# Performance work log

Hardware: AMD Instinct MI355X
Metric: run time of the kernel (lower is better)

The kernel has to match this reference:

```python
import jax, jax.numpy as jnp
import numpy as np

# ---- static config (mirrors init_kwargs) ----
N_DIM = 3                      # manifold dimension n
D_COMP = 6                     # n(n+1)/2 metric components
M_PER = (12, 12, 12)           # HSGP basis functions per dim
M_STAR = 12 * 12 * 12          # 1728
T_STEPS = 50                   # time points in linspace(0,1,t)
C_SCALE = 1.5                  # HSGP domain scaling c
BATCH = 8192
ROWS = np.array([0, 1, 1, 2, 2, 2])   # lower-tri fill order of metric components
COLS = np.array([0, 0, 1, 0, 1, 2])


def _phi_dphi(x, L):
    """HSGP eigenfunctions and their spatial derivatives.
    x: [B, 3], L: [3] -> phi [B, M_STAR], dphi [B, M_STAR, 3]."""
    s, c = [], []
    for d in range(N_DIM):
        k = jnp.arange(1, M_PER[d] + 1, dtype=x.dtype)
        w = jnp.pi * k / (2.0 * L[d])                      # [m_d] frequencies
        arg = w[None, :] * (x[:, d:d + 1] + L[d])          # [B, m_d]
        scale = 1.0 / jnp.sqrt(L[d])
        s.append(scale * jnp.sin(arg))
        c.append(scale * jnp.cos(arg) * w[None, :])
    B = x.shape[0]
    phi = jnp.einsum('bi,bj,bk->bijk', s[0], s[1], s[2]).reshape(B, -1)
    d0 = jnp.einsum('bi,bj,bk->bijk', c[0], s[1], s[2]).reshape(B, -1)
    d1 = jnp.einsum('bi,bj,bk->bijk', s[0], c[1], s[2]).reshape(B, -1)
    d2 = jnp.einsum('bi,bj,bk->bijk', s[0], s[1], c[2]).reshape(B, -1)
    return phi, jnp.stack([d0, d1, d2], axis=-1)


def _omega(L):
    """[M_STAR, 3] angular frequencies of the tensor-product basis."""
    ks = [jnp.arange(1, m + 1, dtype=L.dtype) for m in M_PER]
    kg = jnp.stack(jnp.meshgrid(*ks, indexing='ij'), axis=-1).reshape(-1, N_DIM)
    return jnp.pi * kg / (2.0 * L[None, :])


def _metric_and_grad(x, W, L):
    """Metric g [B,3,3] and its spatial derivative dg [B,3,3,3] (last axis = d/dx_r)."""
    phi, dphi = _phi_dphi(x, L)
    gf = phi @ W.T                                   # [B, 6]
    dgf = jnp.einsum('bmr,dm->bdr', dphi, W)         # [B, 6, 3]
    B = x.shape[0]
    eye = jnp.eye(N_DIM, dtype=x.dtype)
    gl = jnp.zeros((B, N_DIM, N_DIM), x.dtype).at[:, ROWS, COLS].set(gf)
    g = gl + jnp.swapaxes(gl, 1, 2) - gl * eye + eye   # symmetrize + identity offset
    dgl = jnp.zeros((B, N_DIM, N_DIM, N_DIM), x.dtype).at[:, ROWS, COLS, :].set(dgf)
    dg = dgl + jnp.swapaxes(dgl, 1, 2) - dgl * eye[None, :, :, None]
    return g, dg


def _acceleration(pos, vel, W, L):
    """Geodesic equation: a^k = -Gamma^k_{ij} v^i v^j."""
    g, dg = _metric_and_grad(pos, W, L)
    ginv = jnp.linalg.inv(g)
    t1 = jnp.swapaxes(dg, 2, 3)            # [b,l,i,j] = d_i g_{lj}
    t3 = jnp.transpose(dg, (0, 3, 1, 2))   # [b,l,i,j] = d_l g_{ij}
    gamma = 0.5 * jnp.einsum('bkl,blij->bkij', ginv, t1 + dg - t3)
    return -jnp.einsum('bkij,bi,bj->bk', gamma, vel, vel)


def _integrate(pos0, vel0, W, L):
    dt = 1.0 / (T_STEPS - 1)

    def f(p, v):
        return v, _acceleration(p, v, W, L)

    def step(carry, _):
        p, v = carry
        dp1, dv1 = f(p, v)
        dp2, dv2 = f(p + 0.5 * dt * dp1, v + 0.5 * dt * dv1)
        dp3, dv3 = f(p + 0.5 * dt * dp2, v + 0.5 * dt * dv2)
        dp4, dv4 = f(p + dt * dp3, v + dt * dv3)
        pn = p + (dt / 6.0) * (dp1 + 2 * dp2 + 2 * dp3 + dp4)
        vn = v + (dt / 6.0) * (dv1 + 2 * dv2 + 2 * dv3 + dv4)
        return (pn, vn), (pn, vn)

    _, (ps, vs) = jax.lax.scan(step, (pos0, vel0), None, length=T_STEPS - 1)
    pos_traj = jnp.concatenate([pos0[None], ps], axis=0)   # [T, B, 3]
    vel_traj = jnp.concatenate([vel0[None], vs], axis=0)
    return jnp.stack([pos_traj, vel_traj], axis=1)          # [T, 2, B, 3]


def setup_inputs() -> dict:
    key = jax.random.key(0)
    k1, k2, k3, k4, k5 = jax.random.split(key, 5)
    return {
        'pos0': jax.random.normal(k1, (BATCH, N_DIM), jnp.float32),
        'vel0': jax.random.normal(k2, (BATCH, N_DIM), jnp.float32),
        'beta': 0.02 * jax.random.normal(k3, (D_COMP, M_STAR), jnp.float32),
        'ls': 0.5 + jax.random.uniform(k4, (D_COMP, N_DIM), jnp.float32),
        'basis': jax.random.normal(k5, (256, N_DIM), jnp.float32),
    }


def reference(pos0, vel0, beta, ls, basis):
    # HSGP domain half-widths from the linearization anchor points
    L = C_SCALE * jnp.max(jnp.abs(basis), axis=0)           # [3]
    om2 = _omega(L) ** 2                                     # [M_STAR, 3]
    # ExpQuad sqrt spectral density per GP component
    sqrt_psd = ((2.0 * jnp.pi) ** (N_DIM / 4.0)) \
        * jnp.sqrt(jnp.prod(ls, axis=1, keepdims=True)) \
        * jnp.exp(-0.25 * jnp.einsum('mi,di->dm', om2, ls ** 2))  # [6, M_STAR]
    W = beta * sqrt_psd                                      # [6, M_STAR]
    return _integrate(pos0, vel0, W, L)
```

## Files before the change

### kernel.cpp

```cpp
#include <hip/hip_runtime.h>
#include <math.h>

#define BATCH  8192
#define TSTEPS 50
#define PTS    32
#define NTHR   768
#define KSTR   168
#define GKSTR  160
#define TABSTR 100
#define QSTR   5
#define NROW   96
#define PI_F   3.14159265358979323846f

typedef __bf16 bf16x8 __attribute__((ext_vector_type(8)));
typedef float  f32x4  __attribute__((ext_vector_type(4)));

__device__ __forceinline__ unsigned pack2bf(float a, float b) {
    unsigned short ua = __builtin_bit_cast(unsigned short, (__bf16)a);
    unsigned short ub = __builtin_bit_cast(unsigned short, (__bf16)b);
    return (unsigned)ua | ((unsigned)ub << 16);
}

__global__ void precompute_kernel(const float* __restrict__ beta,
                                  const float* __restrict__ ls,
                                  const float* __restrict__ basis,
                                  unsigned short* __restrict__ Wb,
                                  float* __restrict__ auxg)
{
    __shared__ float red[256];
    __shared__ float Ls[3], W1s[3];
    int t = threadIdx.x;

    for (int d = 0; d < 3; ++d) {
        red[t] = fabsf(basis[t*3 + d]);
        __syncthreads();
        for (int s = 128; s > 0; s >>= 1) {
            if (t < s) red[t] = fmaxf(red[t], red[t+s]);
            __syncthreads();
        }
        if (t == 0) {
            float L = 1.5f * red[0];
            Ls[d]  = L;
            W1s[d] = PI_F / (2.0f * L);
        }
        __syncthreads();
    }

    float pref[6], l20[6], l21[6], l22[6];
    #pragma unroll
    for (int dd = 0; dd < 6; ++dd) {
        float a = ls[dd*3+0], b = ls[dd*3+1], c = ls[dd*3+2];
        pref[dd] = 3.9685803f * sqrtf(a*b*c);
        l20[dd] = a*a; l21[dd] = b*b; l22[dd] = c*c;
    }

    for (int idx = t; idx < 96*GKSTR; idx += 256) {
        int n = idx / GKSTR, k = idx - n*GKSTR;
        int d = n >> 4, i = n & 15;
        float v = 0.0f;
        if (i < 12 && k < 144) {
            int j = k / 12, kk = k - (k/12)*12;
            float o0 = W1s[0]*(float)(i+1);
            float o1 = W1s[1]*(float)(j+1);
            float o2 = W1s[2]*(float)(kk+1);
            float e = expf(-0.25f*(o0*o0*l20[d] + o1*o1*l21[d] + o2*o2*l22[d]));
            v = beta[d*1728 + i*144 + k] * pref[d] * e;
        }
        Wb[idx] = __builtin_bit_cast(unsigned short, (__bf16)v);
    }

    if (t < 3) {
        auxg[t]     = Ls[t];
        auxg[3 + t] = W1s[t];
        auxg[6 + t] = 1.0f / sqrtf(Ls[t]);
    }
}

__global__ void __launch_bounds__(NTHR, 3) geodesic_kernel(
    const float* __restrict__ pos0, const float* __restrict__ vel0,
    const unsigned short* __restrict__ Wbg, const float* __restrict__ auxg,
    float* __restrict__ out)
{
    __shared__ __align__(16) __bf16 P[NROW*KSTR];
    __shared__ __align__(16) float tabs[PTS][TABSTR];
    __shared__ __align__(16) float scr[PTS][28];
    __shared__ float qs[PTS][QSTR];

    const int tid = threadIdx.x;

    for (int idx = tid; idx < NROW*KSTR/2; idx += NTHR) ((unsigned*)P)[idx] = 0u;
    if (tid < PTS*8) {
        int zp = tid >> 3, s = tid & 7;
        tabs[zp][(s < 4) ? (12 + s) : (24 + s)] = 0.f;
    }

    float L0 = auxg[0], L1 = auxg[1], L2 = auxg[2];
    float w10 = auxg[3], w11 = auxg[4], w12 = auxg[5];
    float isq0 = auxg[6], isq1 = auxg[7], isq2 = auxg[8];

    const int w = tid >> 6, lane = tid & 63;
    const int nt = w >> 1, mb = (w & 1) * 3;
    const int lrow = lane & 15, lkg = lane >> 4;
    const int nn = nt*16 + lrow;
    const int ptn = nn / 3, pn = nn - 3*ptn;

    bf16x8 wfrag[3][5];
    {
        const __bf16* Wb = (const __bf16*)Wbg;
        #pragma unroll
        for (int mt = 0; mt < 3; ++mt)
            #pragma unroll
            for (int ks = 0; ks < 5; ++ks)
                wfrag[mt][ks] = *(const bf16x8*)(Wb + ((mb+mt)*16 + lrow)*GKSTR + ks*32 + lkg*8);
    }

    const int pt   = tid / 24;
    const int role = tid - pt*24;

    const bool epi_wave = (w < 4);
    const int  myp = (w << 3) + (lane & 7);
    float px=0,py=0,pz=0, vx=0,vy=0,vz=0, vcx=0,vcy=0,vcz=0;
    size_t pg3 = 0;
    if (epi_wave) {
        pg3 = (size_t)(blockIdx.x * PTS + myp) * 3u;
        px = pos0[pg3+0]; py = pos0[pg3+1]; pz = pos0[pg3+2];
        vx = vel0[pg3+0]; vy = vel0[pg3+1]; vz = vel0[pg3+2];
        vcx = vx; vcy = vy; vcz = vz;
        if (lane < 8) {
            qs[myp][0] = px; qs[myp][1] = py; qs[myp][2] = pz;
            out[pg3+0] = px; out[pg3+1] = py; out[pg3+2] = pz;
            out[(size_t)BATCH*3 + pg3 + 0] = vx;
            out[(size_t)BATCH*3 + pg3 + 1] = vy;
            out[(size_t)BATCH*3 + pg3 + 2] = vz;
        }
    }
    __syncthreads();

    const float dt  = 1.0f/49.0f;
    const float hdt = 0.5f/49.0f;
    const float sdt = dt/6.0f;

    #pragma unroll 1
    for (int step = 0; step < TSTEPS-1; ++step) {
        float vsx=0,vsy=0,vsz=0, asx=0,asy=0,asz=0;

        #pragma unroll
        for (int s = 0; s < 4; ++s) {
            if (role < 12) {
                float qx = qs[pt][0], qz = qs[pt][2];
                float sn, cs;
                float wk = w10 * (float)(role+1);
                __sincosf(wk*(qx + L0), &sn, &cs);
                tabs[pt][role]      = isq0*sn;
                tabs[pt][16 + role] = isq0*cs*wk;
                float wk2 = w12 * (float)(role+1);
                __sincosf(wk2*(qz + L2), &sn, &cs);
                tabs[pt][56 + role] = isq2*sn;
                tabs[pt][68 + role] = isq2*cs*wk2;
            } else {
                int kk = role - 12;
                float qy = qs[pt][1];
                float sn, cs;
                float wk = w11 * (float)(kk+1);
                __sincosf(wk*(qy + L1), &sn, &cs);
                tabs[pt][32 + kk] = isq1*sn;
                tabs[pt][44 + kk] = isq1*cs*wk;
            }
            __syncthreads();

            {
                int j = role >> 1, kb = (role & 1)*6;
                float s1 = tabs[pt][32 + j], c1 = tabs[pt][44 + j];
                float2 sa = *(const float2*)&tabs[pt][56 + kb];
                float2 sb = *(const float2*)&tabs[pt][58 + kb];
                float2 sg = *(const float2*)&tabs[pt][60 + kb];
                float2 ca = *(const float2*)&tabs[pt][68 + kb];
                float2 cb = *(const float2*)&tabs[pt][70 + kb];
                float2 cg = *(const float2*)&tabs[pt][72 + kb];
                float s2v[6] = {sa.x, sa.y, sb.x, sb.y, sg.x, sg.y};
                float c2v[6] = {ca.x, ca.y, cb.x, cb.y, cg.x, cg.y};
                int colb = j*12 + kb;
                unsigned* pss = (unsigned*)&P[(pt*3 + 0)*KSTR + colb];
                unsigned* pcs = (unsigned*)&P[(pt*3 + 1)*KSTR + colb];
                unsigned* psc = (unsigned*)&P[(pt*3 + 2)*KSTR + colb];
                #pragma unroll
                for (int u = 0; u < 3; ++u) {
                    pss[u] = pack2bf(s1*s2v[2*u], s1*s2v[2*u+1]);
                    pcs[u] = pack2bf(c1*s2v[2*u], c1*s2v[2*u+1]);
                    psc[u] = pack2bf(s1*c2v[2*u], s1*c2v[2*u+1]);
                }
            }
            __syncthreads();

            f32x4 acc0 = {0.f,0.f,0.f,0.f}, acc1 = {0.f,0.f,0.f,0.f}, acc2 = {0.f,0.f,0.f,0.f};
            #pragma unroll
            for (int ks = 0; ks < 5; ++ks) {
                bf16x8 pf = *(const bf16x8*)&P[nn*KSTR + ks*32 + lkg*8];
                acc0 = __builtin_amdgcn_mfma_f32_16x16x32_bf16(wfrag[0][ks], pf, acc0, 0, 0, 0);
                acc1 = __builtin_amdgcn_mfma_f32_16x16x32_bf16(wfrag[1][ks], pf, acc1, 0, 0, 0);
                acc2 = __builtin_amdgcn_mfma_f32_16x16x32_bf16(wfrag[2][ks], pf, acc2, 0, 0, 0);
            }

            {
                f32x4 s0v = *(const f32x4*)&tabs[ptn][lkg*4];
                f32x4 c0v = *(const f32x4*)&tabs[ptn][16 + lkg*4];

                float vs0 = acc0[0]*s0v[0] + acc0[1]*s0v[1] + acc0[2]*s0v[2] + acc0[3]*s0v[3];
                float vs1 = acc1[0]*s0v[0] + acc1[1]*s0v[1] + acc1[2]*s0v[2] + acc1[3]*s0v[3];
                float vs2 = acc2[0]*s0v[0] + acc2[1]*s0v[1] + acc2[2]*s0v[2] + acc2[3]*s0v[3];
                float vc0 = acc0[0]*c0v[0] + acc0[1]*c0v[1] + acc0[2]*c0v[2] + acc0[3]*c0v[3];
                float vc1 = acc1[0]*c0v[0] + acc1[1]*c0v[1] + acc1[2]*c0v[2] + acc1[3]*c0v[3];
                float vc2 = acc2[0]*c0v[0] + acc2[1]*c0v[1] + acc2[2]*c0v[2] + acc2[3]*c0v[3];

                vs0 += __shfl_xor(vs0, 16); vs0 += __shfl_xor(vs0, 32);
                vs1 += __shfl_xor(vs1, 16); vs1 += __shfl_xor(vs1, 32);
                vs2 += __shfl_xor(vs2, 16); vs2 += __shfl_xor(vs2, 32);
                vc0 += __shfl_xor(vc0, 16); vc0 += __shfl_xor(vc0, 32);
                vc1 += __shfl_xor(vc1, 16); vc1 += __shfl_xor(vc1, 32);
                vc2 += __shfl_xor(vc2, 16); vc2 += __shfl_xor(vc2, 32);

                if (lkg == 0) {
                    int off = (pn == 0) ? 0 : ((pn == 1) ? 12 : 18);
                    scr[ptn][off + mb + 0] = vs0;
                    scr[ptn][off + mb + 1] = vs1;
                    scr[ptn][off + mb + 2] = vs2;
                }
                if (lkg == 1 && pn == 0) {
                    scr[ptn][6 + mb + 0] = vc0;
                    scr[ptn][6 + mb + 1] = vc1;
                    scr[ptn][6 + mb + 2] = vc2;
                }
            }
            __syncthreads();

            if (epi_wave) {
                const f32x4* sp = (const f32x4*)&scr[myp][0];
                f32x4 q0 = sp[0], q1 = sp[1], q2 = sp[2], q3 = sp[3], q4 = sp[4], q5 = sp[5];

                float ux = vcx, uy = vcy, uz = vcz;

                float g00 = q0[0]+1.f, g10 = q0[1], g11 = q0[2]+1.f;
                float g20 = q0[3], g21 = q1[0], g22 = q1[1]+1.f;
                float d0a0=q1[2], d0a1=q1[3], d0a2=q2[0], d0a3=q2[1], d0a4=q2[2], d0a5=q2[3];
                float d1a0=q3[0], d1a1=q3[1], d1a2=q3[2], d1a3=q3[3], d1a4=q4[0], d1a5=q4[1];
                float d2a0=q4[2], d2a1=q4[3], d2a2=q5[0], d2a3=q5[1], d2a4=q5[2], d2a5=q5[3];

                float a00 = g11*g22 - g21*g21;
                float a01 = g20*g21 - g10*g22;
                float a02 = g10*g21 - g20*g11;
                float a11 = g00*g22 - g20*g20;
                float a12 = g10*g20 - g00*g21;
                float a22 = g00*g11 - g10*g10;
                float det = g00*a00 + g10*a01 + g20*a02;
                float inv = 1.0f / det;
                float h00=a00*inv, h01=a01*inv, h02=a02*inv;
                float h11=a11*inv, h12=a12*inv, h22=a22*inv;

                float t0 = ux*d0a0 + uy*d1a0 + uz*d2a0;
                float t1 = ux*d0a1 + uy*d1a1 + uz*d2a1;
                float t2 = ux*d0a2 + uy*d1a2 + uz*d2a2;
                float t3 = ux*d0a3 + uy*d1a3 + uz*d2a3;
                float t4 = ux*d0a4 + uy*d1a4 + uz*d2a4;
                float t5 = ux*d0a5 + uy*d1a5 + uz*d2a5;

                float hl0 = ux*t0 + uy*t1 + uz*t3;
                float hl1 = ux*t1 + uy*t2 + uz*t4;
                float hl2 = ux*t3 + uy*t4 + uz*t5;

                float xx = ux*ux, yy = uy*uy, zz = uz*uz;
                float xy2 = 2.f*ux*uy, xz2 = 2.f*ux*uz, yz2 = 2.f*uy*uz;
                float e0 = xx*d0a0 + xy2*d0a1 + yy*d0a2 + xz2*d0a3 + yz2*d0a4 + zz*d0a5;
                float e1 = xx*d1a0 + xy2*d1a1 + yy*d1a2 + xz2*d1a3 + yz2*d1a4 + zz*d1a5;
                float e2 = xx*d2a0 + xy2*d2a1 + yy*d2a2 + xz2*d2a3 + yz2*d2a4 + zz*d2a5;

                float C0 = hl0 - 0.5f*e0;
                float C1 = hl1 - 0.5f*e1;
                float C2 = hl2 - 0.5f*e2;
                float ax = -(h00*C0 + h01*C1 + h02*C2);
                float ay = -(h01*C0 + h11*C1 + h12*C2);
                float az = -(h02*C0 + h12*C1 + h22*C2);

                const float wgt = (s == 1 || s == 2) ? 2.f : 1.f;
                vsx += wgt*vcx; vsy += wgt*vcy; vsz += wgt*vcz;
                asx += wgt*ax;  asy += wgt*ay;  asz += wgt*az;

                if (s < 3) {
                    const float c = (s == 2) ? dt : hdt;
                    float qnx = fmaf(c, vcx, px);
                    float qny = fmaf(c, vcy, py);
                    float qnz = fmaf(c, vcz, pz);
                    vcx = fmaf(c, ax, vx);
                    vcy = fmaf(c, ay, vy);
                    vcz = fmaf(c, az, vz);
                    if (lane < 8) {
                        qs[myp][0] = qnx; qs[myp][1] = qny; qs[myp][2] = qnz;
                    }
                } else {
                    px = fmaf(sdt, vsx, px);
                    py = fmaf(sdt, vsy, py);
                    pz = fmaf(sdt, vsz, pz);
                    vx = fmaf(sdt, asx, vx);
                    vy = fmaf(sdt, asy, vy);
                    vz = fmaf(sdt, asz, vz);
                    vcx = vx; vcy = vy; vcz = vz;
                    if (lane < 8) {
                        qs[myp][0] = px; qs[myp][1] = py; qs[myp][2] = pz;
                        size_t ob = (size_t)(step+1) * 2u * BATCH * 3u;
                        out[ob + pg3 + 0] = px;
                        out[ob + pg3 + 1] = py;
                        out[ob + pg3 + 2] = pz;
                        out[ob + (size_t)BATCH*3 + pg3 + 0] = vx;
                        out[ob + (size_t)BATCH*3 + pg3 + 1] = vy;
                        out[ob + (size_t)BATCH*3 + pg3 + 2] = vz;
                    }
                }
            }
            __syncthreads();
        }
    }
}

extern "C" void kernel_launch(void* const* d_in, const int* in_sizes, int n_in,
                              void* d_out, int out_size, void* d_ws, size_t ws_size,
                              hipStream_t stream) {
    (void)in_sizes; (void)n_in; (void)out_size; (void)ws_size;
    const float* pos0  = (const float*)d_in[0];
    const float* vel0  = (const float*)d_in[1];
    const float* beta  = (const float*)d_in[2];
    const float* ls    = (const float*)d_in[3];
    const float* basis = (const float*)d_in[4];
    float* outp = (float*)d_out;

    unsigned short* Wb = (unsigned short*)d_ws;
    float* auxg = (float*)((char*)d_ws + 96*GKSTR*sizeof(unsigned short));

    precompute_kernel<<<1, 256, 0, stream>>>(beta, ls, basis, Wb, auxg);
    geodesic_kernel<<<BATCH/PTS, NTHR, 0, stream>>>(pos0, vel0, Wb, auxg, outp);
}
```

Baseline: 419.0 us.

## Make each wavefront own five points and drop block barriers

Each 64-lane wavefront now integrates its own 5 points independently: it computes the sin/cos tables, builds the bf16 basis-product rows, runs all six 16-row MFMA tiles of W itself, and does the Christoffel epilogue. The old 768-thread blocks needed __syncthreads between phases; these are replaced by s_waitcnt lgkmcnt(0) fences within a wave. The cost is 16 MFMA rows holding only 15 useful rows, 6x5 weight fragments kept in registers per wave, and redundant epilogue work on lanes that share a point. Correctness relies on each phase reading only LDS that its own wave wrote.

```diff
diff --git a/kernel.cpp b/kernel.cpp
--- a/kernel.cpp
+++ b/kernel.cpp
@@ -3,17 +3,19 @@
 
 #define BATCH  8192
 #define TSTEPS 50
-#define PTS    32
-#define NTHR   768
+#define WPB    2
+#define PPW    5
 #define KSTR   168
 #define GKSTR  160
 #define TABSTR 100
-#define QSTR   5
-#define NROW   96
 #define PI_F   3.14159265358979323846f
 
 typedef __bf16 bf16x8 __attribute__((ext_vector_type(8)));
 typedef float  f32x4  __attribute__((ext_vector_type(4)));
+
+__device__ __forceinline__ void lds_fence() {
+    asm volatile("s_waitcnt lgkmcnt(0)" ::: "memory");
+}
 
 __device__ __forceinline__ unsigned pack2bf(float a, float b) {
     unsigned short ua = __builtin_bit_cast(unsigned short, (__bf16)a);
@@ -76,65 +78,67 @@
     }
 }
 
-__global__ void __launch_bounds__(NTHR, 3) geodesic_kernel(
+__global__ void __launch_bounds__(64*WPB, 2) geodesic_kernel(
     const float* __restrict__ pos0, const float* __restrict__ vel0,
     const unsigned short* __restrict__ Wbg, const float* __restrict__ auxg,
     float* __restrict__ out)
 {
-    __shared__ __align__(16) __bf16 P[NROW*KSTR];
-    __shared__ __align__(16) float tabs[PTS][TABSTR];
-    __shared__ __align__(16) float scr[PTS][28];
-    __shared__ float qs[PTS][QSTR];
-
-    const int tid = threadIdx.x;
-
-    for (int idx = tid; idx < NROW*KSTR/2; idx += NTHR) ((unsigned*)P)[idx] = 0u;
-    if (tid < PTS*8) {
-        int zp = tid >> 3, s = tid & 7;
-        tabs[zp][(s < 4) ? (12 + s) : (24 + s)] = 0.f;
-    }
-
-    float L0 = auxg[0], L1 = auxg[1], L2 = auxg[2];
-    float w10 = auxg[3], w11 = auxg[4], w12 = auxg[5];
-    float isq0 = auxg[6], isq1 = auxg[7], isq2 = auxg[8];
-
-    const int w = tid >> 6, lane = tid & 63;
-    const int nt = w >> 1, mb = (w & 1) * 3;
+    __shared__ __align__(16) __bf16 Pw[WPB][16*KSTR];
+    __shared__ __align__(16) float tabsw[WPB][PPW][TABSTR];
+    __shared__ __align__(16) float scrw[WPB][16][12];
+    __shared__ float qsw[WPB][PPW][4];
+
+    const int tid  = threadIdx.x;
+    const int wib  = tid >> 6, lane = tid & 63;
+
+    {
+        unsigned* pz = (unsigned*)&Pw[wib][0];
+        for (int i = lane; i < 16*KSTR/2; i += 64) pz[i] = 0u;
+        float* tz = &tabsw[wib][0][0];
+        for (int i = lane; i < PPW*TABSTR; i += 64) tz[i] = 0.f;
+    }
+
+    const float L0 = auxg[0], L1 = auxg[1], L2 = auxg[2];
+    const float w10 = auxg[3], w11 = auxg[4], w12 = auxg[5];
+    const float isq0 = auxg[6], isq1 = auxg[7], isq2 = auxg[8];
+
     const int lrow = lane & 15, lkg = lane >> 4;
-    const int nn = nt*16 + lrow;
-    const int ptn = nn / 3, pn = nn - 3*ptn;
-
-    bf16x8 wfrag[3][5];
+    const int ptl0 = lrow / 3;
+    const int ptl  = (ptl0 > 4) ? 4 : ptl0;
+    const int pn   = lrow - 3*ptl0;
+
+    bf16x8 wfrag[6][5];
     {
         const __bf16* Wb = (const __bf16*)Wbg;
         #pragma unroll
-        for (int mt = 0; mt < 3; ++mt)
+        for (int mt = 0; mt < 6; ++mt)
             #pragma unroll
             for (int ks = 0; ks < 5; ++ks)
-                wfrag[mt][ks] = *(const bf16x8*)(Wb + ((mb+mt)*16 + lrow)*GKSTR + ks*32 + lkg*8);
-    }
-
-    const int pt   = tid / 24;
-    const int role = tid - pt*24;
-
-    const bool epi_wave = (w < 4);
-    const int  myp = (w << 3) + (lane & 7);
-    float px=0,py=0,pz=0, vx=0,vy=0,vz=0, vcx=0,vcy=0,vcz=0;
-    size_t pg3 = 0;
-    if (epi_wave) {
-        pg3 = (size_t)(blockIdx.x * PTS + myp) * 3u;
-        px = pos0[pg3+0]; py = pos0[pg3+1]; pz = pos0[pg3+2];
-        vx = vel0[pg3+0]; vy = vel0[pg3+1]; vz = vel0[pg3+2];
-        vcx = vx; vcy = vy; vcz = vz;
-        if (lane < 8) {
-            qs[myp][0] = px; qs[myp][1] = py; qs[myp][2] = pz;
+                wfrag[mt][ks] = *(const bf16x8*)(Wb + (mt*16 + lrow)*GKSTR + ks*32 + lkg*8);
+    }
+
+    const int wid = blockIdx.x*WPB + wib;
+    const int ptg = wid*PPW + ptl;
+    const bool valid = (ptg < BATCH);
+    const int  ptc = valid ? ptg : (BATCH-1);
+    const size_t pg3 = (size_t)ptg*3;
+
+    float px = pos0[ptc*3+0], py = pos0[ptc*3+1], pz = pos0[ptc*3+2];
+    float vx = vel0[ptc*3+0], vy = vel0[ptc*3+1], vz = vel0[ptc*3+2];
+    float vcx = vx, vcy = vy, vcz = vz;
+
+    const bool qwriter = (pn == 0 && lkg == 0 && lrow < 15);
+
+    if (qwriter) {
+        qsw[wib][ptl][0] = px; qsw[wib][ptl][1] = py; qsw[wib][ptl][2] = pz;
+        if (valid) {
             out[pg3+0] = px; out[pg3+1] = py; out[pg3+2] = pz;
             out[(size_t)BATCH*3 + pg3 + 0] = vx;
             out[(size_t)BATCH*3 + pg3 + 1] = vy;
             out[(size_t)BATCH*3 + pg3 + 2] = vz;
         }
     }
-    __syncthreads();
+    lds_fence();
 
     const float dt  = 1.0f/49.0f;
     const float hdt = 0.5f/49.0f;
@@ -144,117 +148,139 @@
     for (int step = 0; step < TSTEPS-1; ++step) {
         float vsx=0,vsy=0,vsz=0, asx=0,asy=0,asz=0;
 
-        #pragma unroll
+        #pragma unroll 1
         for (int s = 0; s < 4; ++s) {
-            if (role < 12) {
-                float qx = qs[pt][0], qz = qs[pt][2];
+            #pragma unroll 1
+            for (int u = lane; u < 180; u += 64) {
+                int pt = u / 36;
+                int r  = u - 36*pt;
+                int d  = (r < 12) ? 0 : ((r < 24) ? 1 : 2);
+                int k  = r - 12*d;
+                float q   = qsw[wib][pt][d];
+                float Ld  = (d==0)?L0:((d==1)?L1:L2);
+                float w1d = (d==0)?w10:((d==1)?w11:w12);
+                float isd = (d==0)?isq0:((d==1)?isq1:isq2);
+                float wk = w1d * (float)(k+1);
                 float sn, cs;
-                float wk = w10 * (float)(role+1);
-                __sincosf(wk*(qx + L0), &sn, &cs);
-                tabs[pt][role]      = isq0*sn;
-                tabs[pt][16 + role] = isq0*cs*wk;
-                float wk2 = w12 * (float)(role+1);
-                __sincosf(wk2*(qz + L2), &sn, &cs);
-                tabs[pt][56 + role] = isq2*sn;
-                tabs[pt][68 + role] = isq2*cs*wk2;
-            } else {
-                int kk = role - 12;
-                float qy = qs[pt][1];
-                float sn, cs;
-                float wk = w11 * (float)(kk+1);
-                __sincosf(wk*(qy + L1), &sn, &cs);
-                tabs[pt][32 + kk] = isq1*sn;
-                tabs[pt][44 + kk] = isq1*cs*wk;
-            }
-            __syncthreads();
-
-            {
+                __sincosf(wk*(q + Ld), &sn, &cs);
+                int offs = (d==0)?0:((d==1)?32:56);
+                int offc = offs + ((d==0)?16:12);
+                tabsw[wib][pt][offs+k] = isd*sn;
+                tabsw[wib][pt][offc+k] = isd*cs*wk;
+            }
+            lds_fence();
+
+            #pragma unroll 1
+            for (int v = lane; v < 120; v += 64) {
+                int pt = v / 24;
+                int role = v - 24*pt;
                 int j = role >> 1, kb = (role & 1)*6;
-                float s1 = tabs[pt][32 + j], c1 = tabs[pt][44 + j];
-                float2 sa = *(const float2*)&tabs[pt][56 + kb];
-                float2 sb = *(const float2*)&tabs[pt][58 + kb];
-                float2 sg = *(const float2*)&tabs[pt][60 + kb];
-                float2 ca = *(const float2*)&tabs[pt][68 + kb];
-                float2 cb = *(const float2*)&tabs[pt][70 + kb];
-                float2 cg = *(const float2*)&tabs[pt][72 + kb];
+                const float* tb = &tabsw[wib][pt][0];
+                float s1 = tb[32+j], c1 = tb[44+j];
+                float2 sa = *(const float2*)&tb[56+kb];
+                float2 sb = *(const float2*)&tb[58+kb];
+                float2 sg = *(const float2*)&tb[60+kb];
+                float2 ca = *(const float2*)&tb[68+kb];
+                float2 cb = *(const float2*)&tb[70+kb];
+                float2 cg = *(const float2*)&tb[72+kb];
                 float s2v[6] = {sa.x, sa.y, sb.x, sb.y, sg.x, sg.y};
                 float c2v[6] = {ca.x, ca.y, cb.x, cb.y, cg.x, cg.y};
                 int colb = j*12 + kb;
-                unsigned* pss = (unsigned*)&P[(pt*3 + 0)*KSTR + colb];
-                unsigned* pcs = (unsigned*)&P[(pt*3 + 1)*KSTR + colb];
-                unsigned* psc = (unsigned*)&P[(pt*3 + 2)*KSTR + colb];
+                unsigned* pss = (unsigned*)&Pw[wib][(pt*3 + 0)*KSTR + colb];
+                unsigned* pcs = (unsigned*)&Pw[wib][(pt*3 + 1)*KSTR + colb];
+                unsigned* psc = (unsigned*)&Pw[wib][(pt*3 + 2)*KSTR + colb];
                 #pragma unroll
-                for (int u = 0; u < 3; ++u) {
-                    pss[u] = pack2bf(s1*s2v[2*u], s1*s2v[2*u+1]);
-                    pcs[u] = pack2bf(c1*s2v[2*u], c1*s2v[2*u+1]);
-                    psc[u] = pack2bf(s1*c2v[2*u], s1*c2v[2*u+1]);
+                for (int u2 = 0; u2 < 3; ++u2) {
+                    pss[u2] = pack2bf(s1*s2v[2*u2], s1*s2v[2*u2+1]);
+                    pcs[u2] = pack2bf(c1*s2v[2*u2], c1*s2v[2*u2+1]);
+                    psc[u2] = pack2bf(s1*c2v[2*u2], s1*c2v[2*u2+1]);
                 }
             }
-            __syncthreads();
-
-            f32x4 acc0 = {0.f,0.f,0.f,0.f}, acc1 = {0.f,0.f,0.f,0.f}, acc2 = {0.f,0.f,0.f,0.f};
-            #pragma unroll
-            for (int ks = 0; ks < 5; ++ks) {
-                bf16x8 pf = *(const bf16x8*)&P[nn*KSTR + ks*32 + lkg*8];
-                acc0 = __builtin_amdgcn_mfma_f32_16x16x32_bf16(wfrag[0][ks], pf, acc0, 0, 0, 0);
-                acc1 = __builtin_amdgcn_mfma_f32_16x16x32_bf16(wfrag[1][ks], pf, acc1, 0, 0, 0);
-                acc2 = __builtin_amdgcn_mfma_f32_16x16x32_bf16(wfrag[2][ks], pf, acc2, 0, 0, 0);
-            }
-
+            lds_fence();
+
+            f32x4 acc0={0.f,0.f,0.f,0.f}, acc1=acc0, acc2=acc0, acc3=acc0, acc4=acc0, acc5=acc0;
             {
-                f32x4 s0v = *(const f32x4*)&tabs[ptn][lkg*4];
-                f32x4 c0v = *(const f32x4*)&tabs[ptn][16 + lkg*4];
-
+                const __bf16* prow = &Pw[wib][lrow*KSTR];
+                #pragma unroll
+                for (int ks = 0; ks < 5; ++ks) {
+                    bf16x8 pf = *(const bf16x8*)(prow + ks*32 + lkg*8);
+                    acc0 = __builtin_amdgcn_mfma_f32_16x16x32_bf16(wfrag[0][ks], pf, acc0, 0, 0, 0);
+                    acc1 = __builtin_amdgcn_mfma_f32_16x16x32_bf16(wfrag[1][ks], pf, acc1, 0, 0, 0);
+                    acc2 = __builtin_amdgcn_mfma_f32_16x16x32_bf16(wfrag[2][ks], pf, acc2, 0, 0, 0);
+                    acc3 = __builtin_amdgcn_mfma_f32_16x16x32_bf16(wfrag[3][ks], pf, acc3, 0, 0, 0);
+                    acc4 = __builtin_amdgcn_mfma_f32_16x16x32_bf16(wfrag[4][ks], pf, acc4, 0, 0, 0);
+                    acc5 = __builtin_amdgcn_mfma_f32_16x16x32_bf16(wfrag[5][ks], pf, acc5, 0, 0, 0);
+                }
+            }
+
+            {
+                f32x4 s0v = *(const f32x4*)&tabsw[wib][ptl][lkg*4];
+                f32x4 c0v = *(const f32x4*)&tabsw[wib][ptl][16 + lkg*4];
                 float vs0 = acc0[0]*s0v[0] + acc0[1]*s0v[1] + acc0[2]*s0v[2] + acc0[3]*s0v[3];
                 float vs1 = acc1[0]*s0v[0] + acc1[1]*s0v[1] + acc1[2]*s0v[2] + acc1[3]*s0v[3];
                 float vs2 = acc2[0]*s0v[0] + acc2[1]*s0v[1] + acc2[2]*s0v[2] + acc2[3]*s0v[3];
+                float vs3 = acc3[0]*s0v[0] + acc3[1]*s0v[1] + acc3[2]*s0v[2] + acc3[3]*s0v[3];
+                float vs4 = acc4[0]*s0v[0] + acc4[1]*s0v[1] + acc4[2]*s0v[2] + acc4[3]*s0v[3];
+                float vs5 = acc5[0]*s0v[0] + acc5[1]*s0v[1] + acc5[2]*s0v[2] + acc5[3]*s0v[3];
                 float vc0 = acc0[0]*c0v[0] + acc0[1]*c0v[1] + acc0[2]*c0v[2] + acc0[3]*c0v[3];
                 float vc1 = acc1[0]*c0v[0] + acc1[1]*c0v[1] + acc1[2]*c0v[2] + acc1[3]*c0v[3];
                 float vc2 = acc2[0]*c0v[0] + acc2[1]*c0v[1] + acc2[2]*c0v[2] + acc2[3]*c0v[3];
-
-                vs0 += __shfl_xor(vs0, 16); vs0 += __shfl_xor(vs0, 32);
-                vs1 += __shfl_xor(vs1, 16); vs1 += __shfl_xor(vs1, 32);
-                vs2 += __shfl_xor(vs2, 16); vs2 += __shfl_xor(vs2, 32);
-                vc0 += __shfl_xor(vc0, 16); vc0 += __shfl_xor(vc0, 32);
-                vc1 += __shfl_xor(vc1, 16); vc1 += __shfl_xor(vc1, 32);
-                vc2 += __shfl_xor(vc2, 16); vc2 += __shfl_xor(vc2, 32);
+                float vc3 = acc3[0]*c0v[0] + acc3[1]*c0v[1] + acc3[2]*c0v[2] + acc3[3]*c0v[3];
+                float vc4 = acc4[0]*c0v[0] + acc4[1]*c0v[1] + acc4[2]*c0v[2] + acc4[3]*c0v[3];
+                float vc5 = acc5[0]*c0v[0] + acc5[1]*c0v[1] + acc5[2]*c0v[2] + acc5[3]*c0v[3];
+
+                vs0 += __shfl_xor(vs0,16); vs0 += __shfl_xor(vs0,32);
+                vs1 += __shfl_xor(vs1,16); vs1 += __shfl_xor(vs1,32);
+                vs2 += __shfl_xor(vs2,16); vs2 += __shfl_xor(vs2,32);
+                vs3 += __shfl_xor(vs3,16); vs3 += __shfl_xor(vs3,32);
+                vs4 += __shfl_xor(vs4,16); vs4 += __shfl_xor(vs4,32);
+                vs5 += __shfl_xor(vs5,16); vs5 += __shfl_xor(vs5,32);
+                vc0 += __shfl_xor(vc0,16); vc0 += __shfl_xor(vc0,32);
+                vc1 += __shfl_xor(vc1,16); vc1 += __shfl_xor(vc1,32);
+                vc2 += __shfl_xor(vc2,16); vc2 += __shfl_xor(vc2,32);
+                vc3 += __shfl_xor(vc3,16); vc3 += __shfl_xor(vc3,32);
+                vc4 += __shfl_xor(vc4,16); vc4 += __shfl_xor(vc4,32);
+                vc5 += __shfl_xor(vc5,16); vc5 += __shfl_xor(vc5,32);
 
                 if (lkg == 0) {
-                    int off = (pn == 0) ? 0 : ((pn == 1) ? 12 : 18);
-                    scr[ptn][off + mb + 0] = vs0;
-                    scr[ptn][off + mb + 1] = vs1;
-                    scr[ptn][off + mb + 2] = vs2;
+                    float* sr = &scrw[wib][lrow][0];
+                    sr[0]=vs0; sr[1]=vs1; sr[2]=vs2; sr[3]=vs3; sr[4]=vs4; sr[5]=vs5;
+                    sr[6]=vc0; sr[7]=vc1; sr[8]=vc2; sr[9]=vc3; sr[10]=vc4; sr[11]=vc5;
                 }
-                if (lkg == 1 && pn == 0) {
-                    scr[ptn][6 + mb + 0] = vc0;
-                    scr[ptn][6 + mb + 1] = vc1;
-                    scr[ptn][6 + mb + 2] = vc2;
-                }
-            }
-            __syncthreads();
-
-            if (epi_wave) {
-                const f32x4* sp = (const f32x4*)&scr[myp][0];
-                f32x4 q0 = sp[0], q1 = sp[1], q2 = sp[2], q3 = sp[3], q4 = sp[4], q5 = sp[5];
+            }
+            lds_fence();
+
+            float ax, ay, az;
+            {
+                const float* s0p = &scrw[wib][3*ptl    ][0];
+                const float* s1p = &scrw[wib][3*ptl + 1][0];
+                const float* s2p = &scrw[wib][3*ptl + 2][0];
+                f32x4 a0 = *(const f32x4*)&s0p[0];
+                f32x4 a1 = *(const f32x4*)&s0p[4];
+                f32x4 a2 = *(const f32x4*)&s0p[8];
+                f32x4 b0 = *(const f32x4*)&s1p[0];
+                float2 b1 = *(const float2*)&s1p[4];
+                f32x4 c0 = *(const f32x4*)&s2p[0];
+                float2 c1x = *(const float2*)&s2p[4];
 
                 float ux = vcx, uy = vcy, uz = vcz;
 
-                float g00 = q0[0]+1.f, g10 = q0[1], g11 = q0[2]+1.f;
-                float g20 = q0[3], g21 = q1[0], g22 = q1[1]+1.f;
-                float d0a0=q1[2], d0a1=q1[3], d0a2=q2[0], d0a3=q2[1], d0a4=q2[2], d0a5=q2[3];
-                float d1a0=q3[0], d1a1=q3[1], d1a2=q3[2], d1a3=q3[3], d1a4=q4[0], d1a5=q4[1];
-                float d2a0=q4[2], d2a1=q4[3], d2a2=q5[0], d2a3=q5[1], d2a4=q5[2], d2a5=q5[3];
-
-                float a00 = g11*g22 - g21*g21;
-                float a01 = g20*g21 - g10*g22;
-                float a02 = g10*g21 - g20*g11;
-                float a11 = g00*g22 - g20*g20;
-                float a12 = g10*g20 - g00*g21;
-                float a22 = g00*g11 - g10*g10;
-                float det = g00*a00 + g10*a01 + g20*a02;
+                float g00 = a0[0]+1.f, g10 = a0[1], g11 = a0[2]+1.f;
+                float g20 = a0[3], g21 = a1[0], g22 = a1[1]+1.f;
+                float d0a0=a1[2], d0a1=a1[3], d0a2=a2[0], d0a3=a2[1], d0a4=a2[2], d0a5=a2[3];
+                float d1a0=b0[0], d1a1=b0[1], d1a2=b0[2], d1a3=b0[3], d1a4=b1.x, d1a5=b1.y;
+                float d2a0=c0[0], d2a1=c0[1], d2a2=c0[2], d2a3=c0[3], d2a4=c1x.x, d2a5=c1x.y;
+
+                float A00 = g11*g22 - g21*g21;
+                float A01 = g20*g21 - g10*g22;
+                float A02 = g10*g21 - g20*g11;
+                float A11 = g00*g22 - g20*g20;
+                float A12 = g10*g20 - g00*g21;
+                float A22 = g00*g11 - g10*g10;
+                float det = g00*A00 + g10*A01 + g20*A02;
                 float inv = 1.0f / det;
-                float h00=a00*inv, h01=a01*inv, h02=a02*inv;
-                float h11=a11*inv, h12=a12*inv, h22=a22*inv;
+                float h00=A00*inv, h01=A01*inv, h02=A02*inv;
+                float h11=A11*inv, h12=A12*inv, h22=A22*inv;
 
                 float t0 = ux*d0a0 + uy*d1a0 + uz*d2a0;
                 float t1 = ux*d0a1 + uy*d1a1 + uz*d2a1;
@@ -276,10 +302,12 @@
                 float C0 = hl0 - 0.5f*e0;
                 float C1 = hl1 - 0.5f*e1;
                 float C2 = hl2 - 0.5f*e2;
-                float ax = -(h00*C0 + h01*C1 + h02*C2);
-                float ay = -(h01*C0 + h11*C1 + h12*C2);
-                float az = -(h02*C0 + h12*C1 + h22*C2);
-
+                ax = -(h00*C0 + h01*C1 + h02*C2);
+                ay = -(h01*C0 + h11*C1 + h12*C2);
+                az = -(h02*C0 + h12*C1 + h22*C2);
+            }
+
+            {
                 const float wgt = (s == 1 || s == 2) ? 2.f : 1.f;
                 vsx += wgt*vcx; vsy += wgt*vcy; vsz += wgt*vcz;
                 asx += wgt*ax;  asy += wgt*ay;  asz += wgt*az;
@@ -292,8 +320,8 @@
                     vcx = fmaf(c, ax, vx);
                     vcy = fmaf(c, ay, vy);
                     vcz = fmaf(c, az, vz);
-                    if (lane < 8) {
-                        qs[myp][0] = qnx; qs[myp][1] = qny; qs[myp][2] = qnz;
+                    if (qwriter) {
+                        qsw[wib][ptl][0] = qnx; qsw[wib][ptl][1] = qny; qsw[wib][ptl][2] = qnz;
                     }
                 } else {
                     px = fmaf(sdt, vsx, px);
@@ -303,19 +331,21 @@
                     vy = fmaf(sdt, asy, vy);
                     vz = fmaf(sdt, asz, vz);
                     vcx = vx; vcy = vy; vcz = vz;
-                    if (lane < 8) {
-                        qs[myp][0] = px; qs[myp][1] = py; qs[myp][2] = pz;
-                        size_t ob = (size_t)(step+1) * 2u * BATCH * 3u;
-                        out[ob + pg3 + 0] = px;
-                        out[ob + pg3 + 1] = py;
-                        out[ob + pg3 + 2] = pz;
-                        out[ob + (size_t)BATCH*3 + pg3 + 0] = vx;
-                        out[ob + (size_t)BATCH*3 + pg3 + 1] = vy;
-                        out[ob + (size_t)BATCH*3 + pg3 + 2] = vz;
+                    if (qwriter) {
+                        qsw[wib][ptl][0] = px; qsw[wib][ptl][1] = py; qsw[wib][ptl][2] = pz;
+                        if (valid) {
+                            size_t ob = (size_t)(step+1) * 2u * BATCH * 3u;
+                            out[ob + pg3 + 0] = px;
+                            out[ob + pg3 + 1] = py;
+                            out[ob + pg3 + 2] = pz;
+                            out[ob + (size_t)BATCH*3 + pg3 + 0] = vx;
+                            out[ob + (size_t)BATCH*3 + pg3 + 1] = vy;
+                            out[ob + (size_t)BATCH*3 + pg3 + 2] = vz;
+                        }
                     }
                 }
             }
-            __syncthreads();
+            lds_fence();
         }
     }
 }
@@ -335,5 +365,6 @@
     float* auxg = (float*)((char*)d_ws + 96*GKSTR*sizeof(unsigned short));
 
     precompute_kernel<<<1, 256, 0, stream>>>(beta, ls, basis, Wb, auxg);
-    geodesic_kernel<<<BATCH/PTS, NTHR, 0, stream>>>(pos0, vel0, Wb, auxg, outp);
-}
+    const int nblk = (BATCH + WPB*PPW - 1) / (WPB*PPW);
+    geodesic_kernel<<<nblk, 64*WPB, 0, stream>>>(pos0, vel0, Wb, auxg, outp);
+}
```

Result: slower. 522.5 us (+24.7%).

## Add dedicated epilogue waves and spread trig work across 1024 threads

Applied to the files above, without the earlier changes.

Raises the block to 1024 threads. Waves 0-11 do the MFMA GEMM and waves 12-15 become dedicated epilogue/integration waves, where before the first four GEMM waves also did the epilogue. Trig table computation is rebalanced so each thread computes one sin/cos unit, with a small tail handled by the first 128 threads. This aims to shorten the serial epilogue on GEMM waves, but it raises register pressure under the launch_bounds of 4 and adds barrier cost across more threads.

```diff
diff --git a/kernel.cpp b/kernel.cpp
--- a/kernel.cpp
+++ b/kernel.cpp
@@ -4,7 +4,7 @@
 #define BATCH  8192
 #define TSTEPS 50
 #define PTS    32
-#define NTHR   768
+#define NTHR   1024
 #define KSTR   168
 #define GKSTR  160
 #define TABSTR 100
@@ -76,7 +76,29 @@
     }
 }
 
-__global__ void __launch_bounds__(NTHR, 3) geodesic_kernel(
+__device__ __forceinline__ void trig_unit(
+    int u, float (* __restrict__ tabs)[TABSTR], const float (* __restrict__ qs)[QSTR],
+    float L0, float L1, float L2, float w10, float w11, float w12,
+    float isq0, float isq1, float isq2)
+{
+    int pt = u / 36;
+    int r  = u - 36*pt;
+    int d  = (r >= 24) ? 2 : ((r >= 12) ? 1 : 0);
+    int k  = r - 12*d;
+    float q   = qs[pt][d];
+    float Ld  = (d==0)?L0:((d==1)?L1:L2);
+    float w1d = (d==0)?w10:((d==1)?w11:w12);
+    float isd = (d==0)?isq0:((d==1)?isq1:isq2);
+    float wk = w1d * (float)(k+1);
+    float sn, cs;
+    __sincosf(wk*(q + Ld), &sn, &cs);
+    int offs = (d==0)?0:((d==1)?32:56);
+    int offc = offs + ((d==0)?16:12);
+    tabs[pt][offs+k] = isd*sn;
+    tabs[pt][offc+k] = isd*cs*wk;
+}
+
+__global__ void __launch_bounds__(NTHR, 4) geodesic_kernel(
     const float* __restrict__ pos0, const float* __restrict__ vel0,
     const unsigned short* __restrict__ Wbg, const float* __restrict__ auxg,
     float* __restrict__ out)
@@ -94,18 +116,19 @@
         tabs[zp][(s < 4) ? (12 + s) : (24 + s)] = 0.f;
     }
 
-    float L0 = auxg[0], L1 = auxg[1], L2 = auxg[2];
-    float w10 = auxg[3], w11 = auxg[4], w12 = auxg[5];
-    float isq0 = auxg[6], isq1 = auxg[7], isq2 = auxg[8];
+    const float L0 = auxg[0], L1 = auxg[1], L2 = auxg[2];
+    const float w10 = auxg[3], w11 = auxg[4], w12 = auxg[5];
+    const float isq0 = auxg[6], isq1 = auxg[7], isq2 = auxg[8];
 
     const int w = tid >> 6, lane = tid & 63;
     const int nt = w >> 1, mb = (w & 1) * 3;
     const int lrow = lane & 15, lkg = lane >> 4;
     const int nn = nt*16 + lrow;
     const int ptn = nn / 3, pn = nn - 3*ptn;
+    const bool gemm_wave = (w < 12);
 
     bf16x8 wfrag[3][5];
-    {
+    if (gemm_wave) {
         const __bf16* Wb = (const __bf16*)Wbg;
         #pragma unroll
         for (int mt = 0; mt < 3; ++mt)
@@ -114,11 +137,8 @@
                 wfrag[mt][ks] = *(const bf16x8*)(Wb + ((mb+mt)*16 + lrow)*GKSTR + ks*32 + lkg*8);
     }
 
-    const int pt   = tid / 24;
-    const int role = tid - pt*24;
-
-    const bool epi_wave = (w < 4);
-    const int  myp = (w << 3) + (lane & 7);
+    const bool epi_wave = (w >= 12);
+    const int  myp = ((w - 12) << 3) + (lane & 7);
     float px=0,py=0,pz=0, vx=0,vy=0,vz=0, vcx=0,vcy=0,vcz=0;
     size_t pg3 = 0;
     if (epi_wave) {
@@ -146,29 +166,16 @@
 
         #pragma unroll
         for (int s = 0; s < 4; ++s) {
-            if (role < 12) {
-                float qx = qs[pt][0], qz = qs[pt][2];
-                float sn, cs;
-                float wk = w10 * (float)(role+1);
-                __sincosf(wk*(qx + L0), &sn, &cs);
-                tabs[pt][role]      = isq0*sn;
-                tabs[pt][16 + role] = isq0*cs*wk;
-                float wk2 = w12 * (float)(role+1);
-                __sincosf(wk2*(qz + L2), &sn, &cs);
-                tabs[pt][56 + role] = isq2*sn;
-                tabs[pt][68 + role] = isq2*cs*wk2;
-            } else {
-                int kk = role - 12;
-                float qy = qs[pt][1];
-                float sn, cs;
-                float wk = w11 * (float)(kk+1);
-                __sincosf(wk*(qy + L1), &sn, &cs);
-                tabs[pt][32 + kk] = isq1*sn;
-                tabs[pt][44 + kk] = isq1*cs*wk;
-            }
-            __syncthreads();
-
-            {
+            trig_unit(tid, tabs, (const float (*)[QSTR])qs,
+                      L0,L1,L2,w10,w11,w12,isq0,isq1,isq2);
+            if (tid < 128)
+                trig_unit(1024 + tid, tabs, (const float (*)[QSTR])qs,
+                          L0,L1,L2,w10,w11,w12,isq0,isq1,isq2);
+            __syncthreads();
+
+            if (tid < 768) {
+                int pt = tid / 24;
+                int role = tid - pt*24;
                 int j = role >> 1, kb = (role & 1)*6;
                 float s1 = tabs[pt][32 + j], c1 = tabs[pt][44 + j];
                 float2 sa = *(const float2*)&tabs[pt][56 + kb];
@@ -192,16 +199,16 @@
             }
             __syncthreads();
 
-            f32x4 acc0 = {0.f,0.f,0.f,0.f}, acc1 = {0.f,0.f,0.f,0.f}, acc2 = {0.f,0.f,0.f,0.f};
-            #pragma unroll
-            for (int ks = 0; ks < 5; ++ks) {
-                bf16x8 pf = *(const bf16x8*)&P[nn*KSTR + ks*32 + lkg*8];
-                acc0 = __builtin_amdgcn_mfma_f32_16x16x32_bf16(wfrag[0][ks], pf, acc0, 0, 0, 0);
-                acc1 = __builtin_amdgcn_mfma_f32_16x16x32_bf16(wfrag[1][ks], pf, acc1, 0, 0, 0);
-                acc2 = __builtin_amdgcn_mfma_f32_16x16x32_bf16(wfrag[2][ks], pf, acc2, 0, 0, 0);
-            }
-
-            {
+            if (gemm_wave) {
+                f32x4 acc0 = {0.f,0.f,0.f,0.f}, acc1 = {0.f,0.f,0.f,0.f}, acc2 = {0.f,0.f,0.f,0.f};
+                #pragma unroll
+                for (int ks = 0; ks < 5; ++ks) {
+                    bf16x8 pf = *(const bf16x8*)&P[nn*KSTR + ks*32 + lkg*8];
+                    acc0 = __builtin_amdgcn_mfma_f32_16x16x32_bf16(wfrag[0][ks], pf, acc0, 0, 0, 0);
+                    acc1 = __builtin_amdgcn_mfma_f32_16x16x32_bf16(wfrag[1][ks], pf, acc1, 0, 0, 0);
+                    acc2 = __builtin_amdgcn_mfma_f32_16x16x32_bf16(wfrag[2][ks], pf, acc2, 0, 0, 0);
+                }
+
                 f32x4 s0v = *(const f32x4*)&tabs[ptn][lkg*4];
                 f32x4 c0v = *(const f32x4*)&tabs[ptn][16 + lkg*4];
 
```

After: 883.6 us. 111% more time.
